# Kernel optimization log

Measured on AMD Instinct MI355X. Metric: run time of the kernel, lower is better.

Reference implementation:

```python
import jax, jax.numpy as jnp
import numpy as np

Z_RES, N_RES = 128, 512
M_PTS = 2_000_000


def trilinear_devoxelize(grid, coords):
    """Gather-based trilinear interpolation.
    grid:   (Z, N, N, C) voxel grid
    coords: (M, 3) float positions in voxel index space (z, x, y)
    returns (M, C)
    """
    Zd, Nd = grid.shape[0], grid.shape[1]
    c0f = jnp.floor(coords)
    frac = coords - c0f                      # (M, 3) fractional offsets
    maxi = jnp.array([Zd - 1, Nd - 1, Nd - 1], dtype=jnp.int32)
    c0 = jnp.clip(c0f.astype(jnp.int32), 0, maxi)
    c1 = jnp.clip(c0 + 1, 0, maxi)
    fz, fx, fy = frac[:, 0:1], frac[:, 1:2], frac[:, 2:3]
    gz, gx, gy = 1.0 - fz, 1.0 - fx, 1.0 - fy

    def g(zi, xi, yi):
        return grid[zi, xi, yi]              # (M, C) gather

    out = (g(c0[:, 0], c0[:, 1], c0[:, 2]) * gz * gx * gy
         + g(c0[:, 0], c0[:, 1], c1[:, 2]) * gz * gx * fy
         + g(c0[:, 0], c1[:, 1], c0[:, 2]) * gz * fx * gy
         + g(c0[:, 0], c1[:, 1], c1[:, 2]) * gz * fx * fy
         + g(c1[:, 0], c0[:, 1], c0[:, 2]) * fz * gx * gy
         + g(c1[:, 0], c0[:, 1], c1[:, 2]) * fz * gx * fy
         + g(c1[:, 0], c1[:, 1], c0[:, 2]) * fz * fx * gy
         + g(c1[:, 0], c1[:, 1], c1[:, 2]) * fz * fx * fy)
    return out


def setup_inputs() -> dict:
    key = jax.random.key(0)
    k1, k2 = jax.random.split(key)
    extents = jnp.array([Z_RES - 1, N_RES - 1, N_RES - 1], jnp.float32)
    coords = jax.random.uniform(k1, (M_PTS, 3), dtype=jnp.float32) * extents
    # init_scale = 1.0 -> albedo ~ U[0,1); normal initialized to zeros (per module)
    albedo = jax.random.uniform(k2, (Z_RES, N_RES, N_RES), dtype=jnp.float32)
    normal = jnp.zeros((Z_RES, N_RES, N_RES, 3), dtype=jnp.float32)
    return {"coords": coords, "albedo": albedo, "normal": normal}


def reference(coords, albedo, normal):
    base_normal = jnp.array([-1.0, 0.0, 0.0], dtype=jnp.float32)
    a = trilinear_devoxelize(albedo[..., None], coords)[:, 0]   # (M,)
    n = trilinear_devoxelize(normal, coords)                    # (M, 3)
    a = jax.nn.elu(a)
    n = jnp.tanh(n) + base_normal
    # F.normalize(dim=1, eps=1e-12): divide by max(||n||, eps)
    norm = jnp.maximum(jnp.linalg.norm(n, axis=1, keepdims=True), 1e-12)
    n = n / norm
    return (a, n)
```

## Files before the change

### kernel.cpp

```cpp
#include <hip/hip_runtime.h>
#include <math.h>

#define ZR 128
#define NR 512

typedef unsigned int u32x4 __attribute__((ext_vector_type(4)));
typedef unsigned short u16x8 __attribute__((ext_vector_type(8)));


__device__ __forceinline__ float bf16_to_f32(unsigned short u) {
    return __uint_as_float(((unsigned int)u) << 16);
}

__device__ __forceinline__ unsigned short f32_to_bf16_rne(float v) {
    unsigned int u = __float_as_uint(v);
    return (unsigned short)((u + 0x7FFFu + ((u >> 16) & 1u)) >> 16);
}

__device__ __forceinline__ void zcheck_range(
    const u32x4* __restrict__ normal4, long long lo, long long hi,
    long long rank, long long nthreads, unsigned int* __restrict__ flag)
{
    unsigned int acc = 0;
    for (long long i = lo + rank * 256 + threadIdx.x; i < hi; i += nthreads) {
        u32x4 v = __builtin_nontemporal_load(&normal4[i]);
        acc |= v.x | v.y | v.z | v.w;
    }
    if (__ballot(acc != 0) && ((threadIdx.x & 63) == 0))
        atomicOr(flag, 1u);
}

__global__ __launch_bounds__(256) void repack_zcheck_kernel(
    const float* __restrict__ albedo,
    unsigned short* __restrict__ tiled,
    const u32x4* __restrict__ normal4,
    unsigned int* __restrict__ flag,
    long long n4h)
{
    unsigned int b = blockIdx.x;
    if (b < 4096u) {
        zcheck_range(normal4, 0, n4h, (long long)b, 4096LL * 256, flag);
        return;
    }
    unsigned int b2 = b - 4096u;
    int z = (int)(b2 >> 7);
    int xt = (int)(b2 & 127u);

    __shared__ float s[2048];
    const float* src = albedo + ((size_t)z * NR + (size_t)xt * 4) * NR;
    for (int k = threadIdx.x; k < 512; k += 256)
        ((float4*)s)[k] = ((const float4*)src)[k];
    __syncthreads();

    unsigned short* dst = tiled + (size_t)b2 * 2048;
    int t8 = threadIdx.x * 8;
    u16x8 outv;
#pragma unroll
    for (int j = 0; j < 8; j++) {
        int k = t8 + j;
        int yt = k >> 5;
        int r = k & 31;
        int xr = r >> 3;
        int yy = r & 7;
        outv[j] = f32_to_bf16_rne(s[xr * 512 + (yt << 3) + yy]);
    }
    *(u16x8*)(dst + t8) = outv;
}

#define K2_ZBLK 1536
__global__ __launch_bounds__(256) void interp_zcheck_kernel(
    const float* __restrict__ coords,
    const unsigned short* __restrict__ tiled,
    const u32x4* __restrict__ normal4,
    const unsigned int* __restrict__ normal_tail,
    int tail_cnt,
    unsigned int* __restrict__ flag,
    float* __restrict__ out_a,
    float* __restrict__ out_n,
    int M, long long n4h, long long n4)
{
    unsigned int b = blockIdx.x;
    if (b < K2_ZBLK) {
        if (b == 0 && threadIdx.x < (unsigned)tail_cnt) {
            unsigned int tv = normal_tail[threadIdx.x];
            if (tv) atomicOr(flag, 1u);
        }
        zcheck_range(normal4, n4h, n4, (long long)b, (long long)K2_ZBLK * 256, flag);
        return;
    }
    int i = (int)(b - K2_ZBLK) * 256 + threadIdx.x;
    if (i >= M) return;

    float cz = coords[3 * i + 0];
    float cx = coords[3 * i + 1];
    float cy = coords[3 * i + 2];

    float fz0 = floorf(cz), fx0 = floorf(cx), fy0 = floorf(cy);
    float fz = cz - fz0, fx = cx - fx0, fy = cy - fy0;

    int z0 = min(max((int)fz0, 0), ZR - 1);
    int x0 = min(max((int)fx0, 0), NR - 1);
    int y0 = min(max((int)fy0, 0), NR - 1);
    int z1 = min(z0 + 1, ZR - 1);
    int x1 = min(x0 + 1, NR - 1);
    int y1 = min(y0 + 1, NR - 1);

    float gz = 1.0f - fz, gx = 1.0f - fx, gy = 1.0f - fy;

    float w000 = gz * gx * gy, w001 = gz * gx * fy;
    float w010 = gz * fx * gy, w011 = gz * fx * fy;
    float w100 = fz * gx * gy, w101 = fz * gx * fy;
    float w110 = fz * fx * gy, w111 = fz * fx * fy;

    int xo0 = (x0 & 3) << 3, xo1 = (x1 & 3) << 3;
    int yo0 = y0 & 7,        yo1 = y1 & 7;
    int c0 = (y0 >> 3) << 5, c1 = (y1 >> 3) << 5;
    int r00 = ((z0 << 7) + (x0 >> 2)) << 11;
    int r01 = ((z0 << 7) + (x1 >> 2)) << 11;
    int r10 = ((z1 << 7) + (x0 >> 2)) << 11;
    int r11 = ((z1 << 7) + (x1 >> 2)) << 11;

    float a =
        bf16_to_f32(tiled[r00 + c0 + xo0 + yo0]) * w000 +
        bf16_to_f32(tiled[r00 + c1 + xo0 + yo1]) * w001 +
        bf16_to_f32(tiled[r01 + c0 + xo1 + yo0]) * w010 +
        bf16_to_f32(tiled[r01 + c1 + xo1 + yo1]) * w011 +
        bf16_to_f32(tiled[r10 + c0 + xo0 + yo0]) * w100 +
        bf16_to_f32(tiled[r10 + c1 + xo0 + yo1]) * w101 +
        bf16_to_f32(tiled[r11 + c0 + xo1 + yo0]) * w110 +
        bf16_to_f32(tiled[r11 + c1 + xo1 + yo1]) * w111;

    a = (a > 0.0f) ? a : expm1f(a);

    out_a[i] = a;
    out_n[3 * i + 0] = -1.0f;
    out_n[3 * i + 1] = 0.0f;
    out_n[3 * i + 2] = 0.0f;
}

__global__ __launch_bounds__(256) void normal_full_kernel(
    const float* __restrict__ coords,
    const float* __restrict__ normal,
    const unsigned int* __restrict__ flag,
    float* __restrict__ out_n,
    int M)
{
    if (*flag == 0) return;

    int stride = gridDim.x * 256;
    for (int i = blockIdx.x * 256 + threadIdx.x; i < M; i += stride) {
        float cz = coords[3 * i + 0];
        float cx = coords[3 * i + 1];
        float cy = coords[3 * i + 2];

        float fz0 = floorf(cz), fx0 = floorf(cx), fy0 = floorf(cy);
        float fz = cz - fz0, fx = cx - fx0, fy = cy - fy0;

        int z0 = min(max((int)fz0, 0), ZR - 1);
        int x0 = min(max((int)fx0, 0), NR - 1);
        int y0 = min(max((int)fy0, 0), NR - 1);
        int z1 = min(z0 + 1, ZR - 1);
        int x1 = min(x0 + 1, NR - 1);
        int y1 = min(y0 + 1, NR - 1);

        float gz = 1.0f - fz, gx = 1.0f - fx, gy = 1.0f - fy;

        float w000 = gz * gx * gy, w001 = gz * gx * fy;
        float w010 = gz * fx * gy, w011 = gz * fx * fy;
        float w100 = fz * gx * gy, w101 = fz * gx * fy;
        float w110 = fz * fx * gy, w111 = fz * fx * fy;

        size_t b00 = ((size_t)z0 * NR + x0) * NR;
        size_t b01 = ((size_t)z0 * NR + x1) * NR;
        size_t b10 = ((size_t)z1 * NR + x0) * NR;
        size_t b11 = ((size_t)z1 * NR + x1) * NR;

        float n0 = 0.0f, n1 = 0.0f, n2 = 0.0f;
#define ACC(base, yy, w)                                           \
        {                                                          \
            const float* q = normal + ((base) + (size_t)(yy)) * 3; \
            n0 += q[0] * (w);                                      \
            n1 += q[1] * (w);                                      \
            n2 += q[2] * (w);                                      \
        }
        ACC(b00, y0, w000); ACC(b00, y1, w001);
        ACC(b01, y0, w010); ACC(b01, y1, w011);
        ACC(b10, y0, w100); ACC(b10, y1, w101);
        ACC(b11, y0, w110); ACC(b11, y1, w111);
#undef ACC

        n0 = tanhf(n0) - 1.0f;
        n1 = tanhf(n1);
        n2 = tanhf(n2);

        float nrm = sqrtf(n0 * n0 + n1 * n1 + n2 * n2);
        nrm = fmaxf(nrm, 1e-12f);
        float inv = 1.0f / nrm;

        out_n[3 * i + 0] = n0 * inv;
        out_n[3 * i + 1] = n1 * inv;
        out_n[3 * i + 2] = n2 * inv;
    }
}

__global__ __launch_bounds__(256) void devox_direct(
    const float* __restrict__ coords,
    const float* __restrict__ albedo,
    const float* __restrict__ normal,
    float* __restrict__ out_a,
    float* __restrict__ out_n,
    int M)
{
    int i = blockIdx.x * 256 + threadIdx.x;
    if (i >= M) return;

    float cz = coords[3 * i + 0];
    float cx = coords[3 * i + 1];
    float cy = coords[3 * i + 2];

    float fz0 = floorf(cz), fx0 = floorf(cx), fy0 = floorf(cy);
    float fz = cz - fz0, fx = cx - fx0, fy = cy - fy0;

    int z0 = min(max((int)fz0, 0), ZR - 1);
    int x0 = min(max((int)fx0, 0), NR - 1);
    int y0 = min(max((int)fy0, 0), NR - 1);
    int z1 = min(z0 + 1, ZR - 1);
    int x1 = min(x0 + 1, NR - 1);
    int y1 = min(y0 + 1, NR - 1);

    float gz = 1.0f - fz, gx = 1.0f - fx, gy = 1.0f - fy;
    float w000 = gz * gx * gy, w001 = gz * gx * fy;
    float w010 = gz * fx * gy, w011 = gz * fx * fy;
    float w100 = fz * gx * gy, w101 = fz * gx * fy;
    float w110 = fz * fx * gy, w111 = fz * fx * fy;

    size_t b00 = ((size_t)z0 * NR + x0) * NR;
    size_t b01 = ((size_t)z0 * NR + x1) * NR;
    size_t b10 = ((size_t)z1 * NR + x0) * NR;
    size_t b11 = ((size_t)z1 * NR + x1) * NR;

    float a =
        albedo[b00 + y0] * w000 + albedo[b00 + y1] * w001 +
        albedo[b01 + y0] * w010 + albedo[b01 + y1] * w011 +
        albedo[b10 + y0] * w100 + albedo[b10 + y1] * w101 +
        albedo[b11 + y0] * w110 + albedo[b11 + y1] * w111;

    float n0 = 0.0f, n1 = 0.0f, n2 = 0.0f;
#define ACC(base, yy, w)                                           \
    {                                                              \
        const float* q = normal + ((base) + (size_t)(yy)) * 3;     \
        n0 += q[0] * (w);                                          \
        n1 += q[1] * (w);                                          \
        n2 += q[2] * (w);                                          \
    }
    ACC(b00, y0, w000); ACC(b00, y1, w001);
    ACC(b01, y0, w010); ACC(b01, y1, w011);
    ACC(b10, y0, w100); ACC(b10, y1, w101);
    ACC(b11, y0, w110); ACC(b11, y1, w111);
#undef ACC

    a = (a > 0.0f) ? a : expm1f(a);
    n0 = tanhf(n0) - 1.0f;
    n1 = tanhf(n1);
    n2 = tanhf(n2);
    float nrm = sqrtf(n0 * n0 + n1 * n1 + n2 * n2);
    nrm = fmaxf(nrm, 1e-12f);
    float inv = 1.0f / nrm;

    out_a[i] = a;
    out_n[3 * i + 0] = n0 * inv;
    out_n[3 * i + 1] = n1 * inv;
    out_n[3 * i + 2] = n2 * inv;
}

extern "C" void kernel_launch(void* const* d_in, const int* in_sizes, int n_in,
                              void* d_out, int out_size, void* d_ws, size_t ws_size,
                              hipStream_t stream) {
    const float* coords = (const float*)d_in[0];
    const float* albedo = (const float*)d_in[1];
    const float* normal = (const float*)d_in[2];

    int M = in_sizes[0] / 3;
    long long normal_elems = (long long)in_sizes[2];
    long long n4 = normal_elems / 4;
    long long n4h = n4 / 2;
    int tail_cnt = (int)(normal_elems & 3);
    const unsigned int* normal_tail = (const unsigned int*)normal + n4 * 4;

    float* out = (float*)d_out;
    float* out_a = out;
    float* out_n = out + M;

    size_t tiled_off = 256;
    size_t tiled_bytes = (size_t)128 * 128 * 64 * 32 * 2;
    if (ws_size < tiled_off + tiled_bytes) {
        int nblk = (M + 255) / 256;
        devox_direct<<<nblk, 256, 0, stream>>>(coords, albedo, normal, out_a, out_n, M);
        return;
    }

    unsigned int* flag = (unsigned int*)d_ws;
    unsigned short* tiled = (unsigned short*)((char*)d_ws + tiled_off);

    hipMemsetAsync(flag, 0, sizeof(unsigned int), stream);

    repack_zcheck_kernel<<<4096 + 16384, 256, 0, stream>>>(
        albedo, tiled, (const u32x4*)normal, flag, n4h);

    int iblk = (M + 255) / 256;
    interp_zcheck_kernel<<<K2_ZBLK + iblk, 256, 0, stream>>>(
        coords, tiled, (const u32x4*)normal, normal_tail, tail_cnt,
        flag, out_a, out_n, M, n4h, n4);

    normal_full_kernel<<<2048, 256, 0, stream>>>(coords, normal, flag, out_n, M);
}
```

Baseline: 669.8 us.

## Move full normal zero-check into repack kernel with interleaved block roles

The scan that checks whether the normal grid is all zeros now runs entirely inside the repack kernel, using 8192 scan blocks interleaved one-to-two with the 16384 repack blocks so both kinds of work are spread across the GPU. Previously the scan was split, half in the repack kernel and half in the interpolation kernel. The interpolation kernel is now a plain gather kernel with no scan blocks. This aims to balance memory traffic from the two jobs and keep the scan from delaying interpolation, but the whole scan of the normal grid now falls in the first kernel.

```diff
diff --git a/kernel.cpp b/kernel.cpp
--- a/kernel.cpp
+++ b/kernel.cpp
@@ -17,34 +17,38 @@
     return (unsigned short)((u + 0x7FFFu + ((u >> 16) & 1u)) >> 16);
 }
 
-__device__ __forceinline__ void zcheck_range(
-    const u32x4* __restrict__ normal4, long long lo, long long hi,
-    long long rank, long long nthreads, unsigned int* __restrict__ flag)
-{
-    unsigned int acc = 0;
-    for (long long i = lo + rank * 256 + threadIdx.x; i < hi; i += nthreads) {
-        u32x4 v = __builtin_nontemporal_load(&normal4[i]);
-        acc |= v.x | v.y | v.z | v.w;
-    }
-    if (__ballot(acc != 0) && ((threadIdx.x & 63) == 0))
-        atomicOr(flag, 1u);
-}
-
+#define K1_ZBLK 8192
 __global__ __launch_bounds__(256) void repack_zcheck_kernel(
     const float* __restrict__ albedo,
     unsigned short* __restrict__ tiled,
     const u32x4* __restrict__ normal4,
+    const unsigned int* __restrict__ normal_tail,
+    int tail_cnt,
     unsigned int* __restrict__ flag,
-    long long n4h)
+    long long n4)
 {
     unsigned int b = blockIdx.x;
-    if (b < 4096u) {
-        zcheck_range(normal4, 0, n4h, (long long)b, 4096LL * 256, flag);
+    unsigned int g = b / 3u;
+    unsigned int rem = b % 3u;
+
+    if (rem == 0u) {
+        long long zrank = (long long)g;
+        long long nthreads = (long long)K1_ZBLK * 256;
+        unsigned int acc = 0;
+        for (long long i = zrank * 256 + threadIdx.x; i < n4; i += nthreads) {
+            u32x4 v = __builtin_nontemporal_load(&normal4[i]);
+            acc |= v.x | v.y | v.z | v.w;
+        }
+        if (zrank == 0 && threadIdx.x < (unsigned)tail_cnt)
+            acc |= normal_tail[threadIdx.x];
+        if (__ballot(acc != 0) && ((threadIdx.x & 63) == 0))
+            atomicOr(flag, 1u);
         return;
     }
-    unsigned int b2 = b - 4096u;
-    int z = (int)(b2 >> 7);
-    int xt = (int)(b2 & 127u);
+
+    unsigned int r = 2u * g + (rem - 1u);
+    int z = (int)(r >> 7);
+    int xt = (int)(r & 127u);
 
     __shared__ float s[2048];
     const float* src = albedo + ((size_t)z * NR + (size_t)xt * 4) * NR;
@@ -52,43 +56,29 @@
         ((float4*)s)[k] = ((const float4*)src)[k];
     __syncthreads();
 
-    unsigned short* dst = tiled + (size_t)b2 * 2048;
+    unsigned short* dst = tiled + (size_t)r * 2048;
     int t8 = threadIdx.x * 8;
     u16x8 outv;
 #pragma unroll
     for (int j = 0; j < 8; j++) {
         int k = t8 + j;
         int yt = k >> 5;
-        int r = k & 31;
-        int xr = r >> 3;
-        int yy = r & 7;
+        int rr = k & 31;
+        int xr = rr >> 3;
+        int yy = rr & 7;
         outv[j] = f32_to_bf16_rne(s[xr * 512 + (yt << 3) + yy]);
     }
     *(u16x8*)(dst + t8) = outv;
 }
 
-#define K2_ZBLK 1536
-__global__ __launch_bounds__(256) void interp_zcheck_kernel(
+__global__ __launch_bounds__(256) void interp_kernel(
     const float* __restrict__ coords,
     const unsigned short* __restrict__ tiled,
-    const u32x4* __restrict__ normal4,
-    const unsigned int* __restrict__ normal_tail,
-    int tail_cnt,
-    unsigned int* __restrict__ flag,
     float* __restrict__ out_a,
     float* __restrict__ out_n,
-    int M, long long n4h, long long n4)
+    int M)
 {
-    unsigned int b = blockIdx.x;
-    if (b < K2_ZBLK) {
-        if (b == 0 && threadIdx.x < (unsigned)tail_cnt) {
-            unsigned int tv = normal_tail[threadIdx.x];
-            if (tv) atomicOr(flag, 1u);
-        }
-        zcheck_range(normal4, n4h, n4, (long long)b, (long long)K2_ZBLK * 256, flag);
-        return;
-    }
-    int i = (int)(b - K2_ZBLK) * 256 + threadIdx.x;
+    int i = blockIdx.x * 256 + threadIdx.x;
     if (i >= M) return;
 
     float cz = coords[3 * i + 0];
@@ -283,7 +273,6 @@
     int M = in_sizes[0] / 3;
     long long normal_elems = (long long)in_sizes[2];
     long long n4 = normal_elems / 4;
-    long long n4h = n4 / 2;
     int tail_cnt = (int)(normal_elems & 3);
     const unsigned int* normal_tail = (const unsigned int*)normal + n4 * 4;
 
@@ -304,13 +293,11 @@
 
     hipMemsetAsync(flag, 0, sizeof(unsigned int), stream);
 
-    repack_zcheck_kernel<<<4096 + 16384, 256, 0, stream>>>(
-        albedo, tiled, (const u32x4*)normal, flag, n4h);
+    repack_zcheck_kernel<<<3 * K1_ZBLK, 256, 0, stream>>>(
+        albedo, tiled, (const u32x4*)normal, normal_tail, tail_cnt, flag, n4);
 
     int iblk = (M + 255) / 256;
-    interp_zcheck_kernel<<<K2_ZBLK + iblk, 256, 0, stream>>>(
-        coords, tiled, (const u32x4*)normal, normal_tail, tail_cnt,
-        flag, out_a, out_n, M, n4h, n4);
+    interp_kernel<<<iblk, 256, 0, stream>>>(coords, tiled, out_a, out_n, M);
 
     normal_full_kernel<<<2048, 256, 0, stream>>>(coords, normal, flag, out_n, M);
 }
```

After: 693.1 us. +3.5%, slower.
